# Kernel optimization log

Measured on AMD Instinct MI355X. Metric: run time of the kernel, lower is better.

Reference implementation:

```python
import jax, jax.numpy as jnp
import numpy as np

B, D, E, H1, H2 = 64, 2048, 64, 512, 256
EPS = 1e-5


def setup_inputs() -> dict:
    key = jax.random.key(0)
    ks = jax.random.split(key, 8)
    s = lambda k, shape, scale: jax.random.normal(k, shape, dtype=jnp.float32) * scale
    return {
        "sparse_representation": s(ks[0], (B, D), 1.0),
        "emb": s(ks[1], (D, E), 1.0),
        "W1": s(ks[2], (D + E, H1), (D + E) ** -0.5),
        "b1": s(ks[3], (H1,), 0.02),
        "g1": jnp.ones((H1,), jnp.float32),
        "beta1": jnp.zeros((H1,), jnp.float32),
        "m1": jnp.zeros((H1,), jnp.float32),
        "v1": jnp.ones((H1,), jnp.float32),
        "W2": s(ks[4], (H1, H2), H1 ** -0.5),
        "b2": s(ks[5], (H2,), 0.02),
        "g2": jnp.ones((H2,), jnp.float32),
        "beta2": jnp.zeros((H2,), jnp.float32),
        "m2": jnp.zeros((H2,), jnp.float32),
        "v2": jnp.ones((H2,), jnp.float32),
        "W3": s(ks[6], (H2, 1), H2 ** -0.5),
        "b3": s(ks[7], (1,), 0.02),
    }


def _bn_relu(x, g, beta, m, v):
    # eval-mode BatchNorm1d followed by ReLU
    return jax.nn.relu((x - m) * jax.lax.rsqrt(v + EPS) * g + beta)


def reference(sparse_representation, emb, W1, b1, g1, beta1, m1, v1,
              W2, b2, g2, beta2, m2, v2, W3, b3):
    rep = sparse_representation  # (B, D)
    W1d, W1e = W1[:D], W1[D:]    # (D, H1), (E, H1)
    # Fused predict_all: for each k, masked input zeros column k, so
    # Linear(masked_k) = rep @ W1d - rep[:, k] * W1d[k]
    base = rep @ W1d + b1                       # (B, H1)
    emb_h = emb @ W1e                           # (D, H1) per-index embedding contribution
    h1 = base[:, None, :] + emb_h[None, :, :] - rep[:, :, None] * W1d[None, :, :]  # (B, D, H1)
    h1 = _bn_relu(h1, g1, beta1, m1, v1)
    h2 = jnp.einsum("bkh,ho->bko", h1, W2) + b2  # (B, D, H2)
    h2 = _bn_relu(h2, g2, beta2, m2, v2)
    out = jnp.einsum("bkh,h->bk", h2, W3[:, 0]) + b3[0]  # (B, D)
    return out
```

## Files before the change

### kernel.cpp

```cpp
#include <hip/hip_runtime.h>

#define EPS 1e-5f

typedef __attribute__((ext_vector_type(8))) short short8;
typedef __attribute__((ext_vector_type(4))) float f32x4;

__device__ __forceinline__ float bflo(unsigned u) { return __uint_as_float(u << 16); }
__device__ __forceinline__ float bfhi(unsigned u) { return __uint_as_float(u & 0xffff0000u); }
__device__ __forceinline__ unsigned short f2bf(float f) {
  unsigned u = __float_as_uint(f);
  u = u + 0x7FFFu + ((u >> 16) & 1u);
  return (unsigned short)(u >> 16);
}
__device__ __forceinline__ unsigned pack2(float a, float b) {
  return (unsigned)f2bf(a) | ((unsigned)f2bf(b) << 16);
}

__global__ __launch_bounds__(256) void prep(
    const float* __restrict__ emb, const float* __restrict__ W1,
    const float* __restrict__ g1, const float* __restrict__ v1,
    const float* __restrict__ b1, const float* __restrict__ m1,
    const float* __restrict__ beta1,
    const float* __restrict__ W2,
    const float* __restrict__ g2, const float* __restrict__ v2,
    const float* __restrict__ b2, const float* __restrict__ m2,
    const float* __restrict__ beta2,
    unsigned* __restrict__ Q, unsigned* __restrict__ R,
    unsigned short* __restrict__ W2t,
    float* __restrict__ t2, float* __restrict__ c2, float* __restrict__ pbias) {
  const int x = blockIdx.x, t = threadIdx.x;
  if (x < 256) {
    const int k0 = x * 8;
    const int h = t * 2;
    const float a0 = g1[h] * rsqrtf(v1[h] + EPS);
    const float a1 = g1[h + 1] * rsqrtf(v1[h + 1] + EPS);
    const float* We = W1 + 2048 * 512;
    float acc0[8], acc1[8];
    #pragma unroll
    for (int k = 0; k < 8; ++k) { acc0[k] = 0.f; acc1[k] = 0.f; }
    for (int e = 0; e < 64; ++e) {
      float2 wv = *(const float2*)(We + e * 512 + h);
      #pragma unroll
      for (int k = 0; k < 8; ++k) {
        float ev = emb[(k0 + k) * 64 + e];
        acc0[k] = fmaf(ev, wv.x, acc0[k]);
        acc1[k] = fmaf(ev, wv.y, acc1[k]);
      }
    }
    #pragma unroll
    for (int k = 0; k < 8; ++k) {
      Q[(k0 + k) * 256 + t] = pack2(a0 * acc0[k], a1 * acc1[k]);
      float2 wv = *(const float2*)(W1 + (size_t)(k0 + k) * 512 + h);
      R[(k0 + k) * 256 + t] = pack2(a0 * wv.x, a1 * wv.y);
    }
  } else if (x < 320) {
    const int h0 = (x - 256) * 8;
    const int o = t;
    unsigned d[4];
    #pragma unroll
    for (int i = 0; i < 4; ++i) {
      float v0 = W2[(h0 + 2 * i) * 256 + o];
      float v1_ = W2[(h0 + 2 * i + 1) * 256 + o];
      d[i] = pack2(v0, v1_);
    }
    *(uint4*)(W2t + o * 512 + h0) = make_uint4(d[0], d[1], d[2], d[3]);
  } else {
    float tv = g2[t] * rsqrtf(v2[t] + EPS);
    t2[t] = tv;
    c2[t] = tv * (b2[t] - m2[t]) + beta2[t];
    #pragma unroll
    for (int i = 0; i < 2; ++i) {
      int h = t + i * 256;
      float a = g1[h] * rsqrtf(v1[h] + EPS);
      pbias[h] = a * (b1[h] - m1[h]) + beta1[h];
    }
  }
}

__global__ __launch_bounds__(1024) void p_gemm(
    const float* __restrict__ rep, const unsigned* __restrict__ R,
    const float* __restrict__ pbias, unsigned* __restrict__ P) {
  __shared__ float red[16 * 512];
  const int b = blockIdx.x, t = threadIdx.x;
  const int lane = t & 63, kq = t >> 6;
  const int hl = lane * 8;
  const float* rp = rep + b * 2048 + kq * 128;
  const unsigned* Rp = R + (size_t)(kq * 128) * 256 + lane * 4;
  float acc[8];
  #pragma unroll
  for (int i = 0; i < 8; ++i) acc[i] = 0.f;
  #pragma unroll 4
  for (int k = 0; k < 128; ++k) {
    uint4 rv = *(const uint4*)(Rp + (size_t)k * 256);
    float rk = rp[k];
    acc[0] = fmaf(rk, bflo(rv.x), acc[0]); acc[1] = fmaf(rk, bfhi(rv.x), acc[1]);
    acc[2] = fmaf(rk, bflo(rv.y), acc[2]); acc[3] = fmaf(rk, bfhi(rv.y), acc[3]);
    acc[4] = fmaf(rk, bflo(rv.z), acc[4]); acc[5] = fmaf(rk, bfhi(rv.z), acc[5]);
    acc[6] = fmaf(rk, bflo(rv.w), acc[6]); acc[7] = fmaf(rk, bfhi(rv.w), acc[7]);
  }
  *(f32x4*)(&red[kq * 512 + hl])     = (f32x4){acc[0], acc[1], acc[2], acc[3]};
  *(f32x4*)(&red[kq * 512 + hl + 4]) = (f32x4){acc[4], acc[5], acc[6], acc[7]};
  __syncthreads();
  if (t < 256) {
    const int h = t * 2;
    float s0 = 0.f, s1 = 0.f;
    #pragma unroll
    for (int q = 0; q < 16; ++q) { s0 += red[q * 512 + h]; s1 += red[q * 512 + h + 1]; }
    P[b * 256 + t] = pack2(s0 + pbias[h], s1 + pbias[h + 1]);
  }
}

__global__ __launch_bounds__(256, 2) void fused_main(
    const float* __restrict__ rep,
    const unsigned* __restrict__ P,
    const unsigned* __restrict__ Q,
    const unsigned* __restrict__ Rm,
    const unsigned short* __restrict__ W2t,
    const float* __restrict__ t2, const float* __restrict__ c2,
    const float* __restrict__ W3, const float* __restrict__ b3,
    float* __restrict__ out) {
  __shared__ unsigned short A_lds[2][8192];
  __shared__ float repc[128];
  __shared__ float partial[4][128];

  const int t = threadIdx.x;
  const int w = t >> 6;
  const int ln = t & 15;
  const int lq = (t >> 4) & 3;
  const int ks_id = w & 1;
  const int hi_id = w >> 1;
  const int k0 = blockIdx.x * 2;

  if (t < 128) repc[t] = rep[(t & 63) * 2048 + k0 + (t >> 6)];

  f32x4 acc[8][4];
  #pragma unroll
  for (int mi = 0; mi < 8; ++mi)
    #pragma unroll
    for (int nj = 0; nj < 4; ++nj) acc[mi][nj] = (f32x4){0.f, 0.f, 0.f, 0.f};

  __syncthreads();

  auto gen = [&](int c, unsigned short* buf) {
    const int colbase = c * 64 + ks_id * 32 + lq * 8;
    const int cb2 = colbase >> 1;
    #pragma unroll
    for (int p = 0; p < 4; ++p) {
      const int mi = p * 2 + hi_id;
      const int r = mi * 16 + ln;
      const int bb = r & 63;
      const int kg = k0 + (r >> 6);
      uint4 pv = *(const uint4*)(P + (bb << 8) + cb2);
      uint4 qv = *(const uint4*)(Q + (kg << 8) + cb2);
      uint4 rv = *(const uint4*)(Rm + (kg << 8) + cb2);
      const float rb = repc[r];
      unsigned d[4];
      {
        float z0 = fmaf(-rb, bflo(rv.x), bflo(pv.x) + bflo(qv.x));
        float z1 = fmaf(-rb, bfhi(rv.x), bfhi(pv.x) + bfhi(qv.x));
        d[0] = pack2(fmaxf(z0, 0.f), fmaxf(z1, 0.f));
        z0 = fmaf(-rb, bflo(rv.y), bflo(pv.y) + bflo(qv.y));
        z1 = fmaf(-rb, bfhi(rv.y), bfhi(pv.y) + bfhi(qv.y));
        d[1] = pack2(fmaxf(z0, 0.f), fmaxf(z1, 0.f));
        z0 = fmaf(-rb, bflo(rv.z), bflo(pv.z) + bflo(qv.z));
        z1 = fmaf(-rb, bfhi(rv.z), bfhi(pv.z) + bfhi(qv.z));
        d[2] = pack2(fmaxf(z0, 0.f), fmaxf(z1, 0.f));
        z0 = fmaf(-rb, bflo(rv.w), bflo(pv.w) + bflo(qv.w));
        z1 = fmaf(-rb, bfhi(rv.w), bfhi(pv.w) + bfhi(qv.w));
        d[3] = pack2(fmaxf(z0, 0.f), fmaxf(z1, 0.f));
      }
      *(uint4*)(&buf[(size_t)(p * 256 + t) * 8]) = make_uint4(d[0], d[1], d[2], d[3]);
    }
  };

  gen(0, A_lds[0]);

  for (int c = 0; c < 8; ++c) {
    __syncthreads();
    if (c < 7) gen(c + 1, A_lds[(c + 1) & 1]);
    const unsigned short* buf = A_lds[c & 1];
    #pragma unroll
    for (int ks = 0; ks < 2; ++ks) {
      short8 afr[8];
      #pragma unroll
      for (int mi = 0; mi < 8; ++mi)
        afr[mi] = *(const short8*)(buf + (size_t)((((mi * 2 + ks) * 4 + lq) * 16 + ln) * 8));
      short8 bfr[4];
      #pragma unroll
      for (int nj = 0; nj < 4; ++nj)
        bfr[nj] = *(const short8*)(W2t + (size_t)(w * 64 + nj * 16 + ln) * 512 + c * 64 + ks * 32 + lq * 8);
      #pragma unroll
      for (int mi = 0; mi < 8; ++mi)
        #pragma unroll
        for (int nj = 0; nj < 4; ++nj)
          acc[mi][nj] = __builtin_amdgcn_mfma_f32_16x16x32_bf16(afr[mi], bfr[nj], acc[mi][nj], 0, 0, 0);
    }
  }

  float t2v[4], c2v[4], w3v[4];
  #pragma unroll
  for (int nj = 0; nj < 4; ++nj) {
    int o = w * 64 + nj * 16 + ln;
    t2v[nj] = t2[o];
    c2v[nj] = c2[o];
    w3v[nj] = W3[o];
  }
  #pragma unroll
  for (int mi = 0; mi < 8; ++mi) {
    float s[4] = {0.f, 0.f, 0.f, 0.f};
    #pragma unroll
    for (int nj = 0; nj < 4; ++nj)
      #pragma unroll
      for (int r = 0; r < 4; ++r) {
        float u = fmaf(t2v[nj], acc[mi][nj][r], c2v[nj]);
        u = fmaxf(u, 0.f);
        s[r] = fmaf(u, w3v[nj], s[r]);
      }
    #pragma unroll
    for (int r = 0; r < 4; ++r) {
      #pragma unroll
      for (int m = 1; m < 16; m <<= 1) s[r] += __shfl_xor(s[r], m, 64);
    }
    if (ln == 0) {
      #pragma unroll
      for (int r = 0; r < 4; ++r) partial[w][mi * 16 + lq * 4 + r] = s[r];
    }
  }
  __syncthreads();
  if (t < 128) {
    out[(t & 63) * 2048 + k0 + (t >> 6)] =
        partial[0][t] + partial[1][t] + partial[2][t] + partial[3][t] + b3[0];
  }
}

extern "C" void kernel_launch(void* const* d_in, const int* in_sizes, int n_in,
                              void* d_out, int out_size, void* d_ws, size_t ws_size,
                              hipStream_t stream) {
  const float* rep   = (const float*)d_in[0];
  const float* emb   = (const float*)d_in[1];
  const float* W1    = (const float*)d_in[2];
  const float* b1    = (const float*)d_in[3];
  const float* g1    = (const float*)d_in[4];
  const float* beta1 = (const float*)d_in[5];
  const float* m1    = (const float*)d_in[6];
  const float* v1    = (const float*)d_in[7];
  const float* W2    = (const float*)d_in[8];
  const float* b2    = (const float*)d_in[9];
  const float* g2    = (const float*)d_in[10];
  const float* beta2 = (const float*)d_in[11];
  const float* m2    = (const float*)d_in[12];
  const float* v2    = (const float*)d_in[13];
  const float* W3    = (const float*)d_in[14];
  const float* b3    = (const float*)d_in[15];
  float* out = (float*)d_out;

  char* ws = (char*)d_ws;
  float* t2            = (float*)(ws + 0);
  float* c2            = (float*)(ws + 1024);
  float* pbias         = (float*)(ws + 2048);
  unsigned* P          = (unsigned*)(ws + 4096);
  unsigned* Q          = (unsigned*)(ws + 69632);
  unsigned* R          = (unsigned*)(ws + 2166784);
  unsigned short* W2t  = (unsigned short*)(ws + 4263936);

  prep<<<321, 256, 0, stream>>>(emb, W1, g1, v1, b1, m1, beta1, W2, g2, v2, b2, m2,
                                beta2, Q, R, W2t, t2, c2, pbias);
  p_gemm<<<64, 1024, 0, stream>>>(rep, R, pbias, P);
  fused_main<<<1024, 256, 0, stream>>>(rep, P, Q, R, W2t, t2, c2, W3, b3, out);
}
```

Baseline: 194.5 us.

## Build MFMA A-fragments in registers from fp32 chunked P/Q/R, drop LDS staging

The intermediate P, Q and R tensors are now stored as fp32 in a 32-column chunked layout, and W2 is transposed into matching chunks. The main kernel builds each bf16 A fragment directly in registers from P, Q and R and feeds it straight to the MFMAs. This removes the double-buffered LDS staging and the per-chunk barriers. p_gemm now reads fp32 W1 directly and folds in the BN1 bias, and the bf16 pack uses a cheaper perm-based rounding. The cost is more global and L2 traffic from fp32 loads and redundant fragment generation across waves.

```diff
diff --git a/kernel.cpp b/kernel.cpp
--- a/kernel.cpp
+++ b/kernel.cpp
@@ -5,8 +5,6 @@
 typedef __attribute__((ext_vector_type(8))) short short8;
 typedef __attribute__((ext_vector_type(4))) float f32x4;
 
-__device__ __forceinline__ float bflo(unsigned u) { return __uint_as_float(u << 16); }
-__device__ __forceinline__ float bfhi(unsigned u) { return __uint_as_float(u & 0xffff0000u); }
 __device__ __forceinline__ unsigned short f2bf(float f) {
   unsigned u = __float_as_uint(f);
   u = u + 0x7FFFu + ((u >> 16) & 1u);
@@ -19,15 +17,13 @@
 __global__ __launch_bounds__(256) void prep(
     const float* __restrict__ emb, const float* __restrict__ W1,
     const float* __restrict__ g1, const float* __restrict__ v1,
-    const float* __restrict__ b1, const float* __restrict__ m1,
-    const float* __restrict__ beta1,
     const float* __restrict__ W2,
     const float* __restrict__ g2, const float* __restrict__ v2,
     const float* __restrict__ b2, const float* __restrict__ m2,
     const float* __restrict__ beta2,
-    unsigned* __restrict__ Q, unsigned* __restrict__ R,
-    unsigned short* __restrict__ W2t,
-    float* __restrict__ t2, float* __restrict__ c2, float* __restrict__ pbias) {
+    float* __restrict__ Qf, float* __restrict__ Rf,
+    unsigned short* __restrict__ W2f,
+    float* __restrict__ t2, float* __restrict__ c2) {
   const int x = blockIdx.x, t = threadIdx.x;
   if (x < 256) {
     const int k0 = x * 8;
@@ -47,11 +43,14 @@
         acc1[k] = fmaf(ev, wv.y, acc1[k]);
       }
     }
+    const int cs = h >> 5;
+    const int rm = h & 31;
     #pragma unroll
     for (int k = 0; k < 8; ++k) {
-      Q[(k0 + k) * 256 + t] = pack2(a0 * acc0[k], a1 * acc1[k]);
-      float2 wv = *(const float2*)(W1 + (size_t)(k0 + k) * 512 + h);
-      R[(k0 + k) * 256 + t] = pack2(a0 * wv.x, a1 * wv.y);
+      const int kk = k0 + k;
+      *(float2*)(Qf + cs * 65536 + kk * 32 + rm) = make_float2(a0 * acc0[k], a1 * acc1[k]);
+      float2 wv = *(const float2*)(W1 + (size_t)kk * 512 + h);
+      *(float2*)(Rf + cs * 65536 + kk * 32 + rm) = make_float2(a0 * wv.x, a1 * wv.y);
     }
   } else if (x < 320) {
     const int h0 = (x - 256) * 8;
@@ -63,75 +62,101 @@
       float v1_ = W2[(h0 + 2 * i + 1) * 256 + o];
       d[i] = pack2(v0, v1_);
     }
-    *(uint4*)(W2t + o * 512 + h0) = make_uint4(d[0], d[1], d[2], d[3]);
+    const int cs = h0 >> 5;
+    const int rm = h0 & 31;
+    *(uint4*)(W2f + cs * 8192 + o * 32 + rm) = make_uint4(d[0], d[1], d[2], d[3]);
   } else {
     float tv = g2[t] * rsqrtf(v2[t] + EPS);
     t2[t] = tv;
     c2[t] = tv * (b2[t] - m2[t]) + beta2[t];
-    #pragma unroll
-    for (int i = 0; i < 2; ++i) {
-      int h = t + i * 256;
-      float a = g1[h] * rsqrtf(v1[h] + EPS);
-      pbias[h] = a * (b1[h] - m1[h]) + beta1[h];
-    }
   }
 }
 
 __global__ __launch_bounds__(1024) void p_gemm(
-    const float* __restrict__ rep, const unsigned* __restrict__ R,
-    const float* __restrict__ pbias, unsigned* __restrict__ P) {
+    const float* __restrict__ rep, const float* __restrict__ W1,
+    const float* __restrict__ g1, const float* __restrict__ v1,
+    const float* __restrict__ b1, const float* __restrict__ m1,
+    const float* __restrict__ beta1,
+    float* __restrict__ Pf) {
   __shared__ float red[16 * 512];
   const int b = blockIdx.x, t = threadIdx.x;
   const int lane = t & 63, kq = t >> 6;
-  const int hl = lane * 8;
+  const int h = lane * 8;
+  const float* wp = W1 + (size_t)(kq * 128) * 512 + h;
   const float* rp = rep + b * 2048 + kq * 128;
-  const unsigned* Rp = R + (size_t)(kq * 128) * 256 + lane * 4;
   float acc[8];
   #pragma unroll
   for (int i = 0; i < 8; ++i) acc[i] = 0.f;
   #pragma unroll 4
   for (int k = 0; k < 128; ++k) {
-    uint4 rv = *(const uint4*)(Rp + (size_t)k * 256);
+    f32x4 wa = *(const f32x4*)(wp + (size_t)k * 512);
+    f32x4 wb = *(const f32x4*)(wp + (size_t)k * 512 + 4);
     float rk = rp[k];
-    acc[0] = fmaf(rk, bflo(rv.x), acc[0]); acc[1] = fmaf(rk, bfhi(rv.x), acc[1]);
-    acc[2] = fmaf(rk, bflo(rv.y), acc[2]); acc[3] = fmaf(rk, bfhi(rv.y), acc[3]);
-    acc[4] = fmaf(rk, bflo(rv.z), acc[4]); acc[5] = fmaf(rk, bfhi(rv.z), acc[5]);
-    acc[6] = fmaf(rk, bflo(rv.w), acc[6]); acc[7] = fmaf(rk, bfhi(rv.w), acc[7]);
-  }
-  *(f32x4*)(&red[kq * 512 + hl])     = (f32x4){acc[0], acc[1], acc[2], acc[3]};
-  *(f32x4*)(&red[kq * 512 + hl + 4]) = (f32x4){acc[4], acc[5], acc[6], acc[7]};
+    acc[0] = fmaf(rk, wa[0], acc[0]); acc[1] = fmaf(rk, wa[1], acc[1]);
+    acc[2] = fmaf(rk, wa[2], acc[2]); acc[3] = fmaf(rk, wa[3], acc[3]);
+    acc[4] = fmaf(rk, wb[0], acc[4]); acc[5] = fmaf(rk, wb[1], acc[5]);
+    acc[6] = fmaf(rk, wb[2], acc[6]); acc[7] = fmaf(rk, wb[3], acc[7]);
+  }
+  *(f32x4*)(&red[kq * 512 + h])     = (f32x4){acc[0], acc[1], acc[2], acc[3]};
+  *(f32x4*)(&red[kq * 512 + h + 4]) = (f32x4){acc[4], acc[5], acc[6], acc[7]};
   __syncthreads();
-  if (t < 256) {
-    const int h = t * 2;
-    float s0 = 0.f, s1 = 0.f;
-    #pragma unroll
-    for (int q = 0; q < 16; ++q) { s0 += red[q * 512 + h]; s1 += red[q * 512 + h + 1]; }
-    P[b * 256 + t] = pack2(s0 + pbias[h], s1 + pbias[h + 1]);
-  }
+  if (t < 512) {
+    const int hh = t;
+    float tot = 0.f;
+    #pragma unroll
+    for (int q = 0; q < 16; ++q) tot += red[q * 512 + hh];
+    float a = g1[hh] * rsqrtf(v1[hh] + EPS);
+    float val = fmaf(a, tot, fmaf(a, b1[hh] - m1[hh], beta1[hh]));
+    Pf[(hh >> 5) * 2048 + b * 32 + (hh & 31)] = val;
+  }
+}
+
+__device__ __forceinline__ short8 make_frag(f32x4 pa, f32x4 pb,
+                                            f32x4 qa, f32x4 qb,
+                                            f32x4 ra, f32x4 rb_, float rb) {
+  unsigned u[8];
+  #pragma unroll
+  for (int j = 0; j < 4; ++j) {
+    float z0 = fmaf(-rb, ra[j], pa[j] + qa[j]);
+    float z1 = fmaf(-rb, rb_[j], pb[j] + qb[j]);
+    z0 = fmaxf(z0, 0.f);
+    z1 = fmaxf(z1, 0.f);
+    u[j] = __float_as_uint(z0) + 0x8000u;
+    u[j + 4] = __float_as_uint(z1) + 0x8000u;
+  }
+  short8 f;
+  unsigned* fp = (unsigned*)&f;
+  fp[0] = __builtin_amdgcn_perm(u[1], u[0], 0x07060302);
+  fp[1] = __builtin_amdgcn_perm(u[3], u[2], 0x07060302);
+  fp[2] = __builtin_amdgcn_perm(u[5], u[4], 0x07060302);
+  fp[3] = __builtin_amdgcn_perm(u[7], u[6], 0x07060302);
+  return f;
 }
 
 __global__ __launch_bounds__(256, 2) void fused_main(
     const float* __restrict__ rep,
-    const unsigned* __restrict__ P,
-    const unsigned* __restrict__ Q,
-    const unsigned* __restrict__ Rm,
-    const unsigned short* __restrict__ W2t,
+    const float* __restrict__ Pf,
+    const float* __restrict__ Qf,
+    const float* __restrict__ Rf,
+    const unsigned short* __restrict__ W2f,
     const float* __restrict__ t2, const float* __restrict__ c2,
     const float* __restrict__ W3, const float* __restrict__ b3,
     float* __restrict__ out) {
-  __shared__ unsigned short A_lds[2][8192];
-  __shared__ float repc[128];
   __shared__ float partial[4][128];
-
   const int t = threadIdx.x;
   const int w = t >> 6;
   const int ln = t & 15;
   const int lq = (t >> 4) & 3;
-  const int ks_id = w & 1;
-  const int hi_id = w >> 1;
+  const int lqo = lq * 8;
   const int k0 = blockIdx.x * 2;
 
-  if (t < 128) repc[t] = rep[(t & 63) * 2048 + k0 + (t >> 6)];
+  float rbA[4], rbB[4];
+  #pragma unroll
+  for (int pg = 0; pg < 4; ++pg) {
+    float2 rv = *(const float2*)(rep + (pg * 16 + ln) * 2048 + k0);
+    rbA[pg] = rv.x;
+    rbB[pg] = rv.y;
+  }
 
   f32x4 acc[8][4];
   #pragma unroll
@@ -139,61 +164,34 @@
     #pragma unroll
     for (int nj = 0; nj < 4; ++nj) acc[mi][nj] = (f32x4){0.f, 0.f, 0.f, 0.f};
 
-  __syncthreads();
-
-  auto gen = [&](int c, unsigned short* buf) {
-    const int colbase = c * 64 + ks_id * 32 + lq * 8;
-    const int cb2 = colbase >> 1;
-    #pragma unroll
-    for (int p = 0; p < 4; ++p) {
-      const int mi = p * 2 + hi_id;
-      const int r = mi * 16 + ln;
-      const int bb = r & 63;
-      const int kg = k0 + (r >> 6);
-      uint4 pv = *(const uint4*)(P + (bb << 8) + cb2);
-      uint4 qv = *(const uint4*)(Q + (kg << 8) + cb2);
-      uint4 rv = *(const uint4*)(Rm + (kg << 8) + cb2);
-      const float rb = repc[r];
-      unsigned d[4];
-      {
-        float z0 = fmaf(-rb, bflo(rv.x), bflo(pv.x) + bflo(qv.x));
-        float z1 = fmaf(-rb, bfhi(rv.x), bfhi(pv.x) + bfhi(qv.x));
-        d[0] = pack2(fmaxf(z0, 0.f), fmaxf(z1, 0.f));
-        z0 = fmaf(-rb, bflo(rv.y), bflo(pv.y) + bflo(qv.y));
-        z1 = fmaf(-rb, bfhi(rv.y), bfhi(pv.y) + bfhi(qv.y));
-        d[1] = pack2(fmaxf(z0, 0.f), fmaxf(z1, 0.f));
-        z0 = fmaf(-rb, bflo(rv.z), bflo(pv.z) + bflo(qv.z));
-        z1 = fmaf(-rb, bfhi(rv.z), bfhi(pv.z) + bfhi(qv.z));
-        d[2] = pack2(fmaxf(z0, 0.f), fmaxf(z1, 0.f));
-        z0 = fmaf(-rb, bflo(rv.w), bflo(pv.w) + bflo(qv.w));
-        z1 = fmaf(-rb, bfhi(rv.w), bfhi(pv.w) + bfhi(qv.w));
-        d[3] = pack2(fmaxf(z0, 0.f), fmaxf(z1, 0.f));
-      }
-      *(uint4*)(&buf[(size_t)(p * 256 + t) * 8]) = make_uint4(d[0], d[1], d[2], d[3]);
-    }
-  };
-
-  gen(0, A_lds[0]);
-
   for (int c = 0; c < 8; ++c) {
-    __syncthreads();
-    if (c < 7) gen(c + 1, A_lds[(c + 1) & 1]);
-    const unsigned short* buf = A_lds[c & 1];
     #pragma unroll
     for (int ks = 0; ks < 2; ++ks) {
-      short8 afr[8];
-      #pragma unroll
-      for (int mi = 0; mi < 8; ++mi)
-        afr[mi] = *(const short8*)(buf + (size_t)((((mi * 2 + ks) * 4 + lq) * 16 + ln) * 8));
+      const int cs = c * 2 + ks;
+      const float* qb = Qf + cs * 65536 + k0 * 32 + lqo;
+      const float* rp = Rf + cs * 65536 + k0 * 32 + lqo;
+      f32x4 q0a = *(const f32x4*)(qb);      f32x4 q0b = *(const f32x4*)(qb + 4);
+      f32x4 q1a = *(const f32x4*)(qb + 32); f32x4 q1b = *(const f32x4*)(qb + 36);
+      f32x4 r0a = *(const f32x4*)(rp);      f32x4 r0b = *(const f32x4*)(rp + 4);
+      f32x4 r1a = *(const f32x4*)(rp + 32); f32x4 r1b = *(const f32x4*)(rp + 36);
+      const unsigned short* wb = W2f + cs * 8192 + (w * 64 + ln) * 32 + lqo;
       short8 bfr[4];
       #pragma unroll
-      for (int nj = 0; nj < 4; ++nj)
-        bfr[nj] = *(const short8*)(W2t + (size_t)(w * 64 + nj * 16 + ln) * 512 + c * 64 + ks * 32 + lq * 8);
-      #pragma unroll
-      for (int mi = 0; mi < 8; ++mi)
+      for (int nj = 0; nj < 4; ++nj) bfr[nj] = *(const short8*)(wb + nj * 512);
+      const float* pb = Pf + cs * 2048 + ln * 32 + lqo;
+      #pragma unroll
+      for (int pg = 0; pg < 4; ++pg) {
+        f32x4 pa = *(const f32x4*)(pb + pg * 512);
+        f32x4 pc = *(const f32x4*)(pb + pg * 512 + 4);
+        short8 afr = make_frag(pa, pc, q0a, q0b, r0a, r0b, rbA[pg]);
         #pragma unroll
         for (int nj = 0; nj < 4; ++nj)
-          acc[mi][nj] = __builtin_amdgcn_mfma_f32_16x16x32_bf16(afr[mi], bfr[nj], acc[mi][nj], 0, 0, 0);
+          acc[pg][nj] = __builtin_amdgcn_mfma_f32_16x16x32_bf16(afr, bfr[nj], acc[pg][nj], 0, 0, 0);
+        afr = make_frag(pa, pc, q1a, q1b, r1a, r1b, rbB[pg]);
+        #pragma unroll
+        for (int nj = 0; nj < 4; ++nj)
+          acc[pg + 4][nj] = __builtin_amdgcn_mfma_f32_16x16x32_bf16(afr, bfr[nj], acc[pg + 4][nj], 0, 0, 0);
+      }
     }
   }
 
@@ -255,16 +253,15 @@
   float* out = (float*)d_out;
 
   char* ws = (char*)d_ws;
-  float* t2            = (float*)(ws + 0);
-  float* c2            = (float*)(ws + 1024);
-  float* pbias         = (float*)(ws + 2048);
-  unsigned* P          = (unsigned*)(ws + 4096);
-  unsigned* Q          = (unsigned*)(ws + 69632);
-  unsigned* R          = (unsigned*)(ws + 2166784);
-  unsigned short* W2t  = (unsigned short*)(ws + 4263936);
-
-  prep<<<321, 256, 0, stream>>>(emb, W1, g1, v1, b1, m1, beta1, W2, g2, v2, b2, m2,
-                                beta2, Q, R, W2t, t2, c2, pbias);
-  p_gemm<<<64, 1024, 0, stream>>>(rep, R, pbias, P);
-  fused_main<<<1024, 256, 0, stream>>>(rep, P, Q, R, W2t, t2, c2, W3, b3, out);
-}
+  float* t2           = (float*)(ws + 0);
+  float* c2           = (float*)(ws + 1024);
+  float* Pf           = (float*)(ws + 4096);
+  float* Qf           = (float*)(ws + 262144);
+  float* Rf           = (float*)(ws + 4456448);
+  unsigned short* W2f = (unsigned short*)(ws + 8650752);
+
+  prep<<<321, 256, 0, stream>>>(emb, W1, g1, v1, W2, g2, v2, b2, m2, beta2,
+                                Qf, Rf, W2f, t2, c2);
+  p_gemm<<<64, 1024, 0, stream>>>(rep, W1, g1, v1, b1, m1, beta1, Pf);
+  fused_main<<<1024, 256, 0, stream>>>(rep, Pf, Qf, Rf, W2f, t2, c2, W3, b3, out);
+}
```

Measured after the change: 251.7 us. +29.4%, slower.
